# Kernel tuning notes

Measured on AMD Instinct MI355X. Metric: run time of the kernel, lower is better.

The kernel has to match this reference:

```python
import jax, jax.numpy as jnp
import numpy as np

F = 1024
H = 16
DH = F // H  # 64
MLP = 4096
EPS = 1e-5


def layernorm(x, g, b):
    mu = x.mean(-1, keepdims=True)
    var = ((x - mu) ** 2).mean(-1, keepdims=True)
    return (x - mu) * jax.lax.rsqrt(var + EPS) * g + b


def softmax_off_by_one(a):
    e = jnp.exp(a - a.max(-1, keepdims=True))
    return e / (1.0 + e.sum(-1, keepdims=True))


def setup_inputs() -> dict:
    key = jax.random.key(0)
    ks = jax.random.split(key, 12)
    s = 0.02
    return {
        "x": jax.random.normal(ks[0], (2, 2048, F), jnp.float32),
        "ln1_g": jnp.ones((F,), jnp.float32),
        "ln1_b": jnp.zeros((F,), jnp.float32),
        "Wq": jax.random.normal(ks[1], (F, F), jnp.float32) * s,
        "bq": jnp.zeros((F,), jnp.float32),
        "Wk": jax.random.normal(ks[2], (F, F), jnp.float32) * s,
        "bk": jnp.zeros((F,), jnp.float32),
        "Wv": jax.random.normal(ks[3], (F, F), jnp.float32) * s,
        "bv": jnp.zeros((F,), jnp.float32),
        "Wo": jax.random.normal(ks[4], (F, F), jnp.float32) * s,
        "bo": jnp.zeros((F,), jnp.float32),
        "slim": jnp.ones((H,), jnp.float32),
        "ln2_g": jnp.ones((F,), jnp.float32),
        "ln2_b": jnp.zeros((F,), jnp.float32),
        "W1": jax.random.normal(ks[5], (F, MLP), jnp.float32) * s,
        "b1": jnp.zeros((MLP,), jnp.float32),
        "W2": jax.random.normal(ks[6], (MLP, F), jnp.float32) * s,
        "b2": jnp.zeros((F,), jnp.float32),
    }


def reference(x, ln1_g, ln1_b, Wq, bq, Wk, bk, Wv, bv, Wo, bo, slim,
              ln2_g, ln2_b, W1, b1, W2, b2):
    b, n, f = x.shape
    h = layernorm(x, ln1_g, ln1_b)
    # project and split heads: [b, H, n, DH]
    q = (h @ Wq + bq).reshape(b, n, H, DH).transpose(0, 2, 1, 3)
    k = (h @ Wk + bk).reshape(b, n, H, DH).transpose(0, 2, 1, 3)
    v = (h @ Wv + bv).reshape(b, n, H, DH).transpose(0, 2, 1, 3)
    att = jnp.einsum('bhid,bhjd->bhij', q, k) / (DH ** 0.5)
    probs = softmax_off_by_one(att)  # off-by-one softmax
    probs = probs * slim[None, :, None, None]  # slimming after softmax
    attn = jnp.einsum('bhij,bhjd->bihd', probs, v).reshape(b, n, F)
    out = attn @ Wo + bo + x  # residual 1
    h2 = layernorm(out, ln2_g, ln2_b)
    m = jax.nn.gelu(h2 @ W1 + b1, approximate=False)
    m = jax.nn.gelu(m @ W2 + b2, approximate=False)
    return m + out  # residual 2
```

## Files before the change

### kernel.cpp

```cpp
#include <hip/hip_runtime.h>
#include <hip/hip_bf16.h>

typedef __hip_bfloat16 bf16;
typedef short bf16x8 __attribute__((ext_vector_type(8)));
typedef short bf16x4 __attribute__((ext_vector_type(4)));
typedef float f32x4 __attribute__((ext_vector_type(4)));

__device__ __forceinline__ float gelu_f(float x) {
  return 0.5f * x * (1.f + erff(x * 0.70710678118654752f));
}

__device__ __forceinline__ unsigned short f2bfu(float f) {
  bf16 h = __float2bfloat16(f);
  unsigned short u;
  __builtin_memcpy(&u, &h, 2);
  return u;
}

__device__ __forceinline__ void load16_lds(const bf16* g, bf16* l) {
  __builtin_amdgcn_global_load_lds(
      (const __attribute__((address_space(1))) unsigned int*)g,
      (__attribute__((address_space(3))) unsigned int*)l, 16, 0, 0);
}

__global__ __launch_bounds__(256) void transpose_cast(
    const float* __restrict__ src, bf16* __restrict__ dst, int R, int C) {
  __shared__ float tile[32][33];
  int tx = threadIdx.x & 31, ty = threadIdx.x >> 5;
  int r0 = blockIdx.y * 32, c0 = blockIdx.x * 32;
  #pragma unroll
  for (int i = ty; i < 32; i += 8)
    tile[i][tx] = src[(size_t)(r0 + i) * C + (c0 + tx)];
  __syncthreads();
  #pragma unroll
  for (int i = ty; i < 32; i += 8)
    dst[(size_t)(c0 + i) * R + (r0 + tx)] = __float2bfloat16(tile[tx][i]);
}

__global__ __launch_bounds__(256) void ln_kernel(
    const float* __restrict__ x, const float* __restrict__ g,
    const float* __restrict__ b, bf16* __restrict__ y) {
  int row = blockIdx.x;
  int t = threadIdx.x;
  const float4* xr = (const float4*)(x + (size_t)row * 1024);
  float4 v = xr[t];
  float s = v.x + v.y + v.z + v.w;
  float ss = v.x * v.x + v.y * v.y + v.z * v.z + v.w * v.w;
  #pragma unroll
  for (int off = 32; off >= 1; off >>= 1) {
    s += __shfl_xor(s, off);
    ss += __shfl_xor(ss, off);
  }
  __shared__ float red[8];
  int wv = t >> 6;
  if ((t & 63) == 0) { red[wv] = s; red[4 + wv] = ss; }
  __syncthreads();
  float S = red[0] + red[1] + red[2] + red[3];
  float SS = red[4] + red[5] + red[6] + red[7];
  float mu = S * (1.f / 1024.f);
  float var = SS * (1.f / 1024.f) - mu * mu;
  float inv = rsqrtf(var + 1e-5f);
  float4 gv = ((const float4*)g)[t];
  float4 bv = ((const float4*)b)[t];
  ushort4 o;
  o.x = f2bfu((v.x - mu) * inv * gv.x + bv.x);
  o.y = f2bfu((v.y - mu) * inv * gv.y + bv.y);
  o.z = f2bfu((v.z - mu) * inv * gv.z + bv.z);
  o.w = f2bfu((v.w - mu) * inv * gv.w + bv.w);
  ((ushort4*)(y + (size_t)row * 1024))[t] = o;
}

template <int EPI>
__global__ __launch_bounds__(256) void gemm_bf16(
    const bf16* __restrict__ A, const bf16* __restrict__ Bt,
    const float* __restrict__ bias0, const float* __restrict__ resid,
    void* __restrict__ C0, int M, int N, int K) {
  __shared__ __align__(16) bf16 As[2][128 * 32];
  __shared__ __align__(16) bf16 Bs[2][128 * 32];
  const int t = threadIdx.x, lane = t & 63, w = t >> 6;
  const int wm = (w >> 1) * 64, wn = (w & 1) * 64;
  const int m0 = blockIdx.y * 128, n0 = blockIdx.x * 128;

  const int srow = lane >> 2;
  const int sgrp = lane & 3;
  f32x4 acc[4][4] = {};

  const bf16* Abase = A + (size_t)m0 * K;
  const bf16* Bbase = Bt + (size_t)n0 * K;

  auto stage = [&](int buf, int kt) {
    #pragma unroll
    for (int c = 0; c < 2; ++c) {
      int row = w * 32 + c * 16 + srow;
      int sw = (row & 3) ^ ((row >> 2) & 3);
      int gg = sgrp ^ sw;
      const bf16* ga = Abase + (size_t)row * K + kt + gg * 8;
      const bf16* gb = Bbase + (size_t)row * K + kt + gg * 8;
      load16_lds(ga, &As[buf][(w * 32 + c * 16) * 32]);
      load16_lds(gb, &Bs[buf][(w * 32 + c * 16) * 32]);
    }
  };

  const int q8 = (((lane >> 4) ^ (lane & 3) ^ ((lane >> 2) & 3))) * 8;
  const int fr = lane & 15;

  const int nk = K >> 5;
  stage(0, 0);
  for (int i = 0; i < nk; ++i) {
    const int cur = i & 1;
    __syncthreads();
    if (i + 1 < nk) stage(cur ^ 1, (i + 1) << 5);
    bf16x8 af[4], bfr[4];
    #pragma unroll
    for (int mc = 0; mc < 4; ++mc)
      af[mc] = *(const bf16x8*)&As[cur][(wm + mc * 16 + fr) * 32 + q8];
    #pragma unroll
    for (int nc = 0; nc < 4; ++nc)
      bfr[nc] = *(const bf16x8*)&Bs[cur][(wn + nc * 16 + fr) * 32 + q8];
    #pragma unroll
    for (int mc = 0; mc < 4; ++mc)
      #pragma unroll
      for (int nc = 0; nc < 4; ++nc)
        acc[mc][nc] = __builtin_amdgcn_mfma_f32_16x16x32_bf16(
            af[mc], bfr[nc], acc[mc][nc], 0, 0, 0);
  }

  #pragma unroll
  for (int mc = 0; mc < 4; ++mc) {
    #pragma unroll
    for (int reg = 0; reg < 4; ++reg) {
      int m = m0 + wm + mc * 16 + ((lane >> 4) << 2) + reg;
      #pragma unroll
      for (int nc = 0; nc < 4; ++nc) {
        int n = n0 + wn + nc * 16 + (lane & 15);
        float val = acc[mc][nc][reg] + bias0[n];
        size_t idx = (size_t)m * N + n;
        if constexpr (EPI == 3) {
          ((float*)C0)[idx] = val + resid[idx];
        }
      }
    }
  }
}

template <int EPI>
__global__ __launch_bounds__(512, 2) void gemm256(
    const bf16* __restrict__ A, const bf16* __restrict__ Bt,
    const float* __restrict__ bias0, const float* __restrict__ bias1,
    const float* __restrict__ bias2,
    void* __restrict__ C0, void* __restrict__ C1, void* __restrict__ C2,
    int M, int N, int K) {
  __shared__ __align__(16) bf16 As[2][256 * 64];
  __shared__ __align__(16) bf16 Bs[2][256 * 64];
  const int t = threadIdx.x, lane = t & 63, w = t >> 6;
  const int wm = (w >> 2) * 128, wn = (w & 3) * 64;
  const int m0 = blockIdx.y * 256, n0 = blockIdx.x * 256;
  const int koff = (EPI == 6) ? (int)blockIdx.z * 1024 : 0;
  const int nk = ((EPI == 6) ? 1024 : K) >> 6;

  const bf16* Abase = A + (size_t)m0 * K + koff;
  const bf16* Bbase = Bt + (size_t)n0 * K + koff;

  const int lrow = lane >> 3;
  const int lgrp = (lane & 7) ^ lrow;
  const size_t lgoff = (size_t)lrow * K + lgrp * 8;

  auto stageA = [&](int buf, int half, int tile) {
    const int r = half * 128 + w * 16;
    const bf16* g = Abase + (size_t)r * K + tile * 64 + lgoff;
    bf16* l = &As[buf][r * 64];
    load16_lds(g, l);
    load16_lds(g + (size_t)8 * K, l + 8 * 64);
  };
  auto stageB = [&](int buf, int half, int tile) {
    const int r = half * 128 + w * 16;
    const bf16* g = Bbase + (size_t)r * K + tile * 64 + lgoff;
    bf16* l = &Bs[buf][r * 64];
    load16_lds(g, l);
    load16_lds(g + (size_t)8 * K, l + 8 * 64);
  };

  const int fr = lane & 15, qd = lane >> 4, frs = fr & 7;
  const int ao0 = (qd ^ frs) * 8;
  const int ao1 = ((4 + qd) ^ frs) * 8;
  const int rowA = (wm + fr) * 64;
  const int rowB = (wn + fr) * 64;

  f32x4 acc[8][4] = {};
  bf16x8 aF[8][2], bF[4][2];

#define MFMA_Q(MLO, NLO)                                                   \
  _Pragma("unroll")                                                        \
  for (int mi = (MLO); mi < (MLO) + 4; ++mi)                               \
    _Pragma("unroll")                                                      \
    for (int ni = (NLO); ni < (NLO) + 2; ++ni) {                           \
      acc[mi][ni] = __builtin_amdgcn_mfma_f32_16x16x32_bf16(               \
          aF[mi][0], bF[ni][0], acc[mi][ni], 0, 0, 0);                     \
      acc[mi][ni] = __builtin_amdgcn_mfma_f32_16x16x32_bf16(               \
          aF[mi][1], bF[ni][1], acc[mi][ni], 0, 0, 0);                     \
    }

  stageA(0, 0, 0); stageA(0, 1, 0); stageB(0, 0, 0); stageB(0, 1, 0);
  stageA(1, 0, 1);
  asm volatile("s_waitcnt vmcnt(6)" ::: "memory");
  asm volatile("s_barrier" ::: "memory");

  for (int i = 0; i < nk; ++i) {
    const int c = i & 1;
    const bf16* as = &As[c][0];
    const bf16* bs = &Bs[c][0];

    #pragma unroll
    for (int mi = 0; mi < 4; ++mi) {
      aF[mi][0] = *(const bf16x8*)(as + rowA + mi * 1024 + ao0);
      aF[mi][1] = *(const bf16x8*)(as + rowA + mi * 1024 + ao1);
    }
    if (i + 1 < nk) {
      stageA(c ^ 1, 1, i + 1);
      asm volatile("s_waitcnt vmcnt(4)" ::: "memory");
    } else {
      asm volatile("s_waitcnt vmcnt(0)" ::: "memory");
    }
    asm volatile("s_barrier" ::: "memory");
    __builtin_amdgcn_sched_barrier(0);
    if (i) {
      __builtin_amdgcn_s_setprio(1);
      MFMA_Q(4, 2)
      __builtin_amdgcn_s_setprio(0);
    }
    __builtin_amdgcn_sched_barrier(0);
    asm volatile("s_barrier" ::: "memory");

    #pragma unroll
    for (int ni = 0; ni < 2; ++ni) {
      bF[ni][0] = *(const bf16x8*)(bs + rowB + ni * 1024 + ao0);
      bF[ni][1] = *(const bf16x8*)(bs + rowB + ni * 1024 + ao1);
    }
    if (i + 1 < nk) stageB(c ^ 1, 0, i + 1);
    asm volatile("s_barrier" ::: "memory");
    asm volatile("s_waitcnt lgkmcnt(0)" ::: "memory");
    __builtin_amdgcn_sched_barrier(0);
    __builtin_amdgcn_s_setprio(1);
    MFMA_Q(0, 0)
    __builtin_amdgcn_s_setprio(0);
    __builtin_amdgcn_sched_barrier(0);
    asm volatile("s_barrier" ::: "memory");

    #pragma unroll
    for (int mi = 4; mi < 8; ++mi) {
      aF[mi][0] = *(const bf16x8*)(as + rowA + mi * 1024 + ao0);
      aF[mi][1] = *(const bf16x8*)(as + rowA + mi * 1024 + ao1);
    }
    if (i + 1 < nk) stageB(c ^ 1, 1, i + 1);
    asm volatile("s_barrier" ::: "memory");
    asm volatile("s_waitcnt lgkmcnt(0)" ::: "memory");
    __builtin_amdgcn_sched_barrier(0);
    __builtin_amdgcn_s_setprio(1);
    MFMA_Q(4, 0)
    __builtin_amdgcn_s_setprio(0);
    __builtin_amdgcn_sched_barrier(0);
    asm volatile("s_barrier" ::: "memory");

    #pragma unroll
    for (int ni = 2; ni < 4; ++ni) {
      bF[ni][0] = *(const bf16x8*)(bs + rowB + ni * 1024 + ao0);
      bF[ni][1] = *(const bf16x8*)(bs + rowB + ni * 1024 + ao1);
    }
    if (i + 2 < nk) stageA(c, 0, i + 2);
    if (i + 1 < nk) {
      if (i + 2 < nk) {
        asm volatile("s_waitcnt vmcnt(6)" ::: "memory");
      } else {
        asm volatile("s_waitcnt vmcnt(4)" ::: "memory");
      }
    }
    asm volatile("s_barrier" ::: "memory");
    asm volatile("s_waitcnt lgkmcnt(0)" ::: "memory");
    __builtin_amdgcn_sched_barrier(0);
    __builtin_amdgcn_s_setprio(1);
    MFMA_Q(0, 2)
    __builtin_amdgcn_s_setprio(0);
    __builtin_amdgcn_sched_barrier(0);
    asm volatile("s_barrier" ::: "memory");
  }
  MFMA_Q(4, 2)
#undef MFMA_Q

  if constexpr (EPI == 0) {
    const int which = n0 >> 10;
    const float* bp = which == 0 ? bias0 : which == 1 ? bias1 : bias2;
    bf16* qk = (bf16*)(which == 0 ? C0 : C1);
    const float qscale = 0.18033688011112042f;
    #pragma unroll
    for (int mi = 0; mi < 8; ++mi) {
      #pragma unroll
      for (int reg = 0; reg < 4; ++reg) {
        int m = m0 + wm + mi * 16 + qd * 4 + reg;
        int b = m >> 11, tok = m & 2047;
        #pragma unroll
        for (int ni = 0; ni < 4; ++ni) {
          int n = n0 + wn + ni * 16 + fr;
          int nn = n & 1023, hh = nn >> 6, d = n & 63;
          float val = acc[mi][ni][reg] + bp[nn];
          if (which == 2)
            ((bf16*)C2)[(size_t)((b * 16 + hh) * 64 + d) * 2048 + tok] =
                __float2bfloat16(val);
          else if (which == 0)
            qk[(size_t)((b * 16 + hh) * 2048 + tok) * 64 + d] =
                __float2bfloat16(val * qscale);
          else
            qk[(size_t)((b * 16 + hh) * 2048 + tok) * 64 + d] =
                __float2bfloat16(val);
        }
      }
    }
  } else if constexpr (EPI == 4) {
    #pragma unroll
    for (int mi = 0; mi < 8; ++mi) {
      #pragma unroll
      for (int reg = 0; reg < 4; ++reg) {
        int m = m0 + wm + mi * 16 + qd * 4 + reg;
        #pragma unroll
        for (int ni = 0; ni < 4; ++ni) {
          int n = n0 + wn + ni * 16 + fr;
          float val = acc[mi][ni][reg] + bias0[n];
          ((bf16*)C0)[(size_t)m * N + n] = __float2bfloat16(gelu_f(val));
        }
      }
    }
  } else {
    bf16* pout = (bf16*)C0 + (size_t)blockIdx.z * M * N;
    #pragma unroll
    for (int mi = 0; mi < 8; ++mi) {
      #pragma unroll
      for (int reg = 0; reg < 4; ++reg) {
        int m = m0 + wm + mi * 16 + qd * 4 + reg;
        #pragma unroll
        for (int ni = 0; ni < 4; ++ni) {
          int n = n0 + wn + ni * 16 + fr;
          pout[(size_t)m * N + n] = __float2bfloat16(acc[mi][ni][reg]);
        }
      }
    }
  }
}

__global__ __launch_bounds__(256) void reduce_mlp2(
    const bf16* __restrict__ part, const float* __restrict__ b2,
    const float* __restrict__ out1, float* __restrict__ out) {
  const int row = blockIdx.x, t = threadIdx.x;
  const size_t base = (size_t)row * 1024 + t * 4;
  float sum[4] = {0.f, 0.f, 0.f, 0.f};
  #pragma unroll
  for (int kc = 0; kc < 4; ++kc) {
    ushort4 u = *(const ushort4*)(part + (size_t)kc * 4096 * 1024 + base);
    unsigned short us[4] = {u.x, u.y, u.z, u.w};
    #pragma unroll
    for (int j = 0; j < 4; ++j) {
      bf16 h;
      __builtin_memcpy(&h, &us[j], 2);
      sum[j] += __bfloat162float(h);
    }
  }
  float4 bv = ((const float4*)b2)[t];
  float4 rv = *(const float4*)(out1 + base);
  float4 o;
  o.x = gelu_f(sum[0] + bv.x) + rv.x;
  o.y = gelu_f(sum[1] + bv.y) + rv.y;
  o.z = gelu_f(sum[2] + bv.z) + rv.z;
  o.w = gelu_f(sum[3] + bv.w) + rv.w;
  *(float4*)(out + base) = o;
}

__global__ __launch_bounds__(256) void attn_kernel(
    const bf16* __restrict__ q, const bf16* __restrict__ k,
    const bf16* __restrict__ vt, const float* __restrict__ slim,
    bf16* __restrict__ attn) {
  __shared__ __align__(16) bf16 Ks[64][72];
  __shared__ __align__(16) bf16 Vs[64][72];
  __shared__ __align__(16) bf16 Ps[4][2][16][72];

  const int t = threadIdx.x, lane = t & 63, w = t >> 6;
  const int fr = lane & 15, qd = lane >> 4;
  const int bh = blockIdx.y;
  const int q0 = blockIdx.x * 128;
  const size_t bhbase = (size_t)bh * 2048 * 64;

  bf16x8 qf[2][2];
  #pragma unroll
  for (int s = 0; s < 2; ++s) {
    const int qrow = q0 + s * 64 + w * 16 + fr;
    const bf16* qp = q + bhbase + (size_t)qrow * 64 + qd * 8;
    qf[s][0] = *(const bf16x8*)qp;
    qf[s][1] = *(const bf16x8*)(qp + 32);
  }

  const int r0 = t >> 3, g0 = t & 7;
  const bf16* kbase = k + bhbase + (size_t)r0 * 64 + g0 * 8;
  const bf16* vbase = vt + bhbase + (size_t)r0 * 2048 + g0 * 8;

  bf16x8 kreg0, kreg1, vreg0, vreg1;
  auto gload = [&](int j0) {
    kreg0 = *(const bf16x8*)(kbase + (size_t)j0 * 64);
    kreg1 = *(const bf16x8*)(kbase + (size_t)(j0 + 32) * 64);
    vreg0 = *(const bf16x8*)(vbase + j0);
    vreg1 = *(const bf16x8*)(vbase + (size_t)32 * 2048 + j0);
  };
  gload(0);

  f32x4 o_acc[2][4] = {};
  float m4[2][4] = {};
  float l4[2][4] = {};

  for (int it = 0; it < 32; ++it) {
    *(bf16x8*)&Ks[r0][g0 * 8] = kreg0;
    *(bf16x8*)&Ks[r0 + 32][g0 * 8] = kreg1;
    *(bf16x8*)&Vs[r0][g0 * 8] = vreg0;
    *(bf16x8*)&Vs[r0 + 32][g0 * 8] = vreg1;
    __syncthreads();
    if (it + 1 < 32) gload((it + 1) * 64);

    bf16x8 kf[4][2];
    #pragma unroll
    for (int nc = 0; nc < 4; ++nc) {
      int kr = nc * 16 + fr;
      kf[nc][0] = *(const bf16x8*)&Ks[kr][qd * 8];
      kf[nc][1] = *(const bf16x8*)&Ks[kr][32 + qd * 8];
    }

    f32x4 z[2][4];
    #pragma unroll
    for (int s = 0; s < 2; ++s)
      #pragma unroll
      for (int nc = 0; nc < 4; ++nc) {
        f32x4 zz = {};
        zz = __builtin_amdgcn_mfma_f32_16x16x32_bf16(kf[nc][0], qf[s][0], zz, 0, 0, 0);
        zz = __builtin_amdgcn_mfma_f32_16x16x32_bf16(kf[nc][1], qf[s][1], zz, 0, 0, 0);
        z[s][nc] = zz;
      }

    bf16x8 vf[4][2];
    #pragma unroll
    for (int dc = 0; dc < 4; ++dc) {
      int vr = dc * 16 + fr;
      vf[dc][0] = *(const bf16x8*)&Vs[vr][qd * 8];
      vf[dc][1] = *(const bf16x8*)&Vs[vr][32 + qd * 8];
    }

    #pragma unroll
    for (int s = 0; s < 2; ++s) {
      #pragma unroll
      for (int nc = 0; nc < 4; ++nc) {
        float p0 = __builtin_amdgcn_exp2f(z[s][nc][0]);
        float p1 = __builtin_amdgcn_exp2f(z[s][nc][1]);
        float p2 = __builtin_amdgcn_exp2f(z[s][nc][2]);
        float p3 = __builtin_amdgcn_exp2f(z[s][nc][3]);
        l4[s][nc] += (p0 + p1) + (p2 + p3);
        m4[s][nc] = fmaxf(m4[s][nc], fmaxf(fmaxf(p0, p1), fmaxf(p2, p3)));
        bf16x4 pk;
        pk[0] = (short)f2bfu(p0);
        pk[1] = (short)f2bfu(p1);
        pk[2] = (short)f2bfu(p2);
        pk[3] = (short)f2bfu(p3);
        *(bf16x4*)&Ps[w][s][fr][nc * 16 + qd * 4] = pk;
      }

      bf16x8 pf0 = *(const bf16x8*)&Ps[w][s][fr][qd * 8];
      bf16x8 pf1 = *(const bf16x8*)&Ps[w][s][fr][32 + qd * 8];
      #pragma unroll
      for (int dc = 0; dc < 4; ++dc) {
        o_acc[s][dc] = __builtin_amdgcn_mfma_f32_16x16x32_bf16(pf0, vf[dc][0], o_acc[s][dc], 0, 0, 0);
        o_acc[s][dc] = __builtin_amdgcn_mfma_f32_16x16x32_bf16(pf1, vf[dc][1], o_acc[s][dc], 0, 0, 0);
      }
    }
    __syncthreads();
  }

  const int b = bh >> 4, hh = bh & 15;
  const float sl = slim[hh];
  #pragma unroll
  for (int s = 0; s < 2; ++s) {
    float l_all = (l4[s][0] + l4[s][1]) + (l4[s][2] + l4[s][3]);
    float m_all = fmaxf(fmaxf(m4[s][0], m4[s][1]), fmaxf(m4[s][2], m4[s][3]));
    l_all += __shfl_xor(l_all, 16);
    m_all = fmaxf(m_all, __shfl_xor(m_all, 16));
    l_all += __shfl_xor(l_all, 32);
    m_all = fmaxf(m_all, __shfl_xor(m_all, 32));

    #pragma unroll
    for (int r = 0; r < 4; ++r) {
      float lr = __shfl(l_all, qd * 4 + r);
      float mr = __shfl(m_all, qd * 4 + r);
      float inv = sl / (mr + lr);
      int mrow = b * 2048 + q0 + s * 64 + w * 16 + qd * 4 + r;
      #pragma unroll
      for (int dc = 0; dc < 4; ++dc) {
        int col = hh * 64 + dc * 16 + fr;
        attn[(size_t)mrow * 1024 + col] = __float2bfloat16(o_acc[s][dc][r] * inv);
      }
    }
  }
}

extern "C" void kernel_launch(void* const* d_in, const int* in_sizes, int n_in,
                              void* d_out, int out_size, void* d_ws, size_t ws_size,
                              hipStream_t stream) {
  const float* x    = (const float*)d_in[0];
  const float* ln1g = (const float*)d_in[1];
  const float* ln1b = (const float*)d_in[2];
  const float* Wq   = (const float*)d_in[3];
  const float* bq   = (const float*)d_in[4];
  const float* Wk   = (const float*)d_in[5];
  const float* bk   = (const float*)d_in[6];
  const float* Wv   = (const float*)d_in[7];
  const float* bv   = (const float*)d_in[8];
  const float* Wo   = (const float*)d_in[9];
  const float* bo   = (const float*)d_in[10];
  const float* slim = (const float*)d_in[11];
  const float* ln2g = (const float*)d_in[12];
  const float* ln2b = (const float*)d_in[13];
  const float* W1   = (const float*)d_in[14];
  const float* b1   = (const float*)d_in[15];
  const float* W2   = (const float*)d_in[16];
  const float* b2   = (const float*)d_in[17];

  char* p = (char*)d_ws;
  auto take = [&](size_t nbytes) {
    char* r = p;
    p += (nbytes + 255) & ~(size_t)255;
    return r;
  };
  bf16* Wqkv_t = (bf16*)take((size_t)3072 * 1024 * 2);
  bf16* Wo_t = (bf16*)take((size_t)1024 * 1024 * 2);
  bf16* W1_t = (bf16*)take((size_t)4096 * 1024 * 2);
  bf16* W2_t = (bf16*)take((size_t)1024 * 4096 * 2);
  bf16* h1   = (bf16*)take((size_t)4096 * 1024 * 2);
  bf16* qb   = (bf16*)take((size_t)4096 * 1024 * 2);
  bf16* kb   = (bf16*)take((size_t)4096 * 1024 * 2);
  bf16* vtb  = (bf16*)take((size_t)4096 * 1024 * 2);
  bf16* attn = (bf16*)take((size_t)4096 * 1024 * 2);
  float* out1 = (float*)take((size_t)4096 * 1024 * 4);
  bf16* h2   = (bf16*)take((size_t)4096 * 1024 * 2);
  bf16* m1   = (bf16*)take((size_t)4096 * 4096 * 2);

  bf16* parts = h1;

  dim3 blk(256);
  dim3 blk512(512);

  transpose_cast<<<dim3(32, 32), blk, 0, stream>>>(Wq, Wqkv_t, 1024, 1024);
  transpose_cast<<<dim3(32, 32), blk, 0, stream>>>(Wk, Wqkv_t + (size_t)1024 * 1024, 1024, 1024);
  transpose_cast<<<dim3(32, 32), blk, 0, stream>>>(Wv, Wqkv_t + (size_t)2048 * 1024, 1024, 1024);
  transpose_cast<<<dim3(32, 32), blk, 0, stream>>>(Wo, Wo_t, 1024, 1024);
  transpose_cast<<<dim3(128, 32), blk, 0, stream>>>(W1, W1_t, 1024, 4096);
  transpose_cast<<<dim3(32, 128), blk, 0, stream>>>(W2, W2_t, 4096, 1024);

  ln_kernel<<<4096, blk, 0, stream>>>(x, ln1g, ln1b, h1);

  gemm256<0><<<dim3(12, 16), blk512, 0, stream>>>(
      h1, Wqkv_t, bq, bk, bv, qb, kb, vtb, 4096, 3072, 1024);

  attn_kernel<<<dim3(16, 32), blk, 0, stream>>>(qb, kb, vtb, slim, attn);

  gemm_bf16<3><<<dim3(8, 32), blk, 0, stream>>>(
      attn, Wo_t, bo, x, out1, 4096, 1024, 1024);

  ln_kernel<<<4096, blk, 0, stream>>>(out1, ln2g, ln2b, h2);

  gemm256<4><<<dim3(16, 16), blk512, 0, stream>>>(
      h2, W1_t, b1, nullptr, nullptr, m1, nullptr, nullptr, 4096, 4096, 1024);

  gemm256<6><<<dim3(4, 16, 4), blk512, 0, stream>>>(
      m1, W2_t, nullptr, nullptr, nullptr, parts, nullptr, nullptr,
      4096, 1024, 4096);
  reduce_mlp2<<<4096, blk, 0, stream>>>(parts, b2, out1, (float*)d_out);
}
```

Before: 406.3 us.

## Double-buffer K/V tiles via direct global-to-LDS loads with XOR swizzle

The attention kernel now stages K and V tiles straight from global memory into LDS with global_load_lds, using a two-slot ring so the next tile loads while the current one is being computed. It also drops one barrier per iteration and stops routing the data through registers. Row padding is replaced by an XOR chunk swizzle that keeps LDS reads conflict-free in the smaller layout. s_setprio is raised around the MFMA blocks so compute waves get issue priority. The risk is correctness if the async LDS writes are not fully waited on before the barrier.

```diff
diff --git a/kernel.cpp b/kernel.cpp
--- a/kernel.cpp
+++ b/kernel.cpp
@@ -376,8 +376,8 @@
     const bf16* __restrict__ q, const bf16* __restrict__ k,
     const bf16* __restrict__ vt, const float* __restrict__ slim,
     bf16* __restrict__ attn) {
-  __shared__ __align__(16) bf16 Ks[64][72];
-  __shared__ __align__(16) bf16 Vs[64][72];
+  __shared__ __align__(16) bf16 Ks[2][64][64];
+  __shared__ __align__(16) bf16 Vs[2][64][64];
   __shared__ __align__(16) bf16 Ps[4][2][16][72];
 
   const int t = threadIdx.x, lane = t & 63, w = t >> 6;
@@ -395,40 +395,44 @@
     qf[s][1] = *(const bf16x8*)(qp + 32);
   }
 
-  const int r0 = t >> 3, g0 = t & 7;
-  const bf16* kbase = k + bhbase + (size_t)r0 * 64 + g0 * 8;
-  const bf16* vbase = vt + bhbase + (size_t)r0 * 2048 + g0 * 8;
-
-  bf16x8 kreg0, kreg1, vreg0, vreg1;
-  auto gload = [&](int j0) {
-    kreg0 = *(const bf16x8*)(kbase + (size_t)j0 * 64);
-    kreg1 = *(const bf16x8*)(kbase + (size_t)(j0 + 32) * 64);
-    vreg0 = *(const bf16x8*)(vbase + j0);
-    vreg1 = *(const bf16x8*)(vbase + (size_t)32 * 2048 + j0);
+  const int rw = lane >> 3, sl = lane & 7;
+  const int gsw = (sl ^ rw) * 8;
+  auto stageKV = [&](int buf, int key0) {
+    #pragma unroll
+    for (int c = 0; c < 2; ++c) {
+      const int row0 = c * 32 + w * 8;
+      const bf16* gk = k + bhbase + (size_t)(key0 + row0 + rw) * 64 + gsw;
+      const bf16* gv = vt + bhbase + (size_t)(row0 + rw) * 2048 + key0 + gsw;
+      load16_lds(gk, &Ks[buf][row0][0]);
+      load16_lds(gv, &Vs[buf][row0][0]);
+    }
   };
-  gload(0);
+  stageKV(0, 0);
 
   f32x4 o_acc[2][4] = {};
   float m4[2][4] = {};
   float l4[2][4] = {};
 
+  const int frs = fr & 7;
+  const int so0 = (qd ^ frs) * 8;
+  const int so1 = ((4 + qd) ^ frs) * 8;
+
+  __syncthreads();
+
   for (int it = 0; it < 32; ++it) {
-    *(bf16x8*)&Ks[r0][g0 * 8] = kreg0;
-    *(bf16x8*)&Ks[r0 + 32][g0 * 8] = kreg1;
-    *(bf16x8*)&Vs[r0][g0 * 8] = vreg0;
-    *(bf16x8*)&Vs[r0 + 32][g0 * 8] = vreg1;
-    __syncthreads();
-    if (it + 1 < 32) gload((it + 1) * 64);
+    const int cur = it & 1;
+    if (it + 1 < 32) stageKV(cur ^ 1, (it + 1) * 64);
 
     bf16x8 kf[4][2];
     #pragma unroll
     for (int nc = 0; nc < 4; ++nc) {
-      int kr = nc * 16 + fr;
-      kf[nc][0] = *(const bf16x8*)&Ks[kr][qd * 8];
-      kf[nc][1] = *(const bf16x8*)&Ks[kr][32 + qd * 8];
+      const bf16* kr = &Ks[cur][nc * 16 + fr][0];
+      kf[nc][0] = *(const bf16x8*)(kr + so0);
+      kf[nc][1] = *(const bf16x8*)(kr + so1);
     }
 
     f32x4 z[2][4];
+    __builtin_amdgcn_s_setprio(1);
     #pragma unroll
     for (int s = 0; s < 2; ++s)
       #pragma unroll
@@ -438,13 +442,14 @@
         zz = __builtin_amdgcn_mfma_f32_16x16x32_bf16(kf[nc][1], qf[s][1], zz, 0, 0, 0);
         z[s][nc] = zz;
       }
+    __builtin_amdgcn_s_setprio(0);
 
     bf16x8 vf[4][2];
     #pragma unroll
     for (int dc = 0; dc < 4; ++dc) {
-      int vr = dc * 16 + fr;
-      vf[dc][0] = *(const bf16x8*)&Vs[vr][qd * 8];
-      vf[dc][1] = *(const bf16x8*)&Vs[vr][32 + qd * 8];
+      const bf16* vr = &Vs[cur][dc * 16 + fr][0];
+      vf[dc][0] = *(const bf16x8*)(vr + so0);
+      vf[dc][1] = *(const bf16x8*)(vr + so1);
     }
 
     #pragma unroll
@@ -467,17 +472,19 @@
 
       bf16x8 pf0 = *(const bf16x8*)&Ps[w][s][fr][qd * 8];
       bf16x8 pf1 = *(const bf16x8*)&Ps[w][s][fr][32 + qd * 8];
+      __builtin_amdgcn_s_setprio(1);
       #pragma unroll
       for (int dc = 0; dc < 4; ++dc) {
         o_acc[s][dc] = __builtin_amdgcn_mfma_f32_16x16x32_bf16(pf0, vf[dc][0], o_acc[s][dc], 0, 0, 0);
         o_acc[s][dc] = __builtin_amdgcn_mfma_f32_16x16x32_bf16(pf1, vf[dc][1], o_acc[s][dc], 0, 0, 0);
       }
+      __builtin_amdgcn_s_setprio(0);
     }
     __syncthreads();
   }
 
   const int b = bh >> 4, hh = bh & 15;
-  const float sl = slim[hh];
+  const float sl_f = slim[hh];
   #pragma unroll
   for (int s = 0; s < 2; ++s) {
     float l_all = (l4[s][0] + l4[s][1]) + (l4[s][2] + l4[s][3]);
@@ -491,7 +498,7 @@
     for (int r = 0; r < 4; ++r) {
       float lr = __shfl(l_all, qd * 4 + r);
       float mr = __shfl(m_all, qd * 4 + r);
-      float inv = sl / (mr + lr);
+      float inv = sl_f / (mr + lr);
       int mrow = b * 2048 + q0 + s * 64 + w * 16 + qd * 4 + r;
       #pragma unroll
       for (int dc = 0; dc < 4; ++dc) {
```

Result: slower. 417.5 us (+2.8%).

## Load K/V fragments directly from global into registers, dropping LDS staging

Applied to the files above, without the earlier changes.

The attention kernel stops staging K and V tiles through shared memory with block-wide barriers. Each wave now loads its MFMA operand fragments straight from global memory into double-buffered registers, and the next tile's K and V loads are issued around the current tile's matrix ops. It also adds s_setprio around the MFMA sections and sets launch bounds to one block per SM. The goal is to remove LDS round trips and __syncthreads stalls. The cost is that each of the four waves now fetches the same K/V data from global/L2 redundantly, and register pressure rises, which may lower occupancy.

```diff
diff --git a/kernel.cpp b/kernel.cpp
--- a/kernel.cpp
+++ b/kernel.cpp
@@ -372,12 +372,10 @@
   *(float4*)(out + base) = o;
 }
 
-__global__ __launch_bounds__(256) void attn_kernel(
+__global__ __launch_bounds__(256, 1) void attn_kernel(
     const bf16* __restrict__ q, const bf16* __restrict__ k,
     const bf16* __restrict__ vt, const float* __restrict__ slim,
     bf16* __restrict__ attn) {
-  __shared__ __align__(16) bf16 Ks[64][72];
-  __shared__ __align__(16) bf16 Vs[64][72];
   __shared__ __align__(16) bf16 Ps[4][2][16][72];
 
   const int t = threadIdx.x, lane = t & 63, w = t >> 6;
@@ -395,89 +393,93 @@
     qf[s][1] = *(const bf16x8*)(qp + 32);
   }
 
-  const int r0 = t >> 3, g0 = t & 7;
-  const bf16* kbase = k + bhbase + (size_t)r0 * 64 + g0 * 8;
-  const bf16* vbase = vt + bhbase + (size_t)r0 * 2048 + g0 * 8;
-
-  bf16x8 kreg0, kreg1, vreg0, vreg1;
-  auto gload = [&](int j0) {
-    kreg0 = *(const bf16x8*)(kbase + (size_t)j0 * 64);
-    kreg1 = *(const bf16x8*)(kbase + (size_t)(j0 + 32) * 64);
-    vreg0 = *(const bf16x8*)(vbase + j0);
-    vreg1 = *(const bf16x8*)(vbase + (size_t)32 * 2048 + j0);
-  };
-  gload(0);
+  const bf16* kfb = k + bhbase + (size_t)fr * 64 + qd * 8;
+  const bf16* vfb = vt + bhbase + (size_t)fr * 2048 + qd * 8;
+
+  bf16x8 kR[2][4][2], vR[2][4][2];
+
+#define ISSUE_K(SL, KEY0)                                                     \
+  _Pragma("unroll")                                                           \
+  for (int nc = 0; nc < 4; ++nc) {                                            \
+    const bf16* kp_ = kfb + (size_t)((KEY0) + nc * 16) * 64;                  \
+    kR[SL][nc][0] = *(const bf16x8*)kp_;                                      \
+    kR[SL][nc][1] = *(const bf16x8*)(kp_ + 32);                               \
+  }
+
+#define ISSUE_V(SL, KEY0)                                                     \
+  _Pragma("unroll")                                                           \
+  for (int dc = 0; dc < 4; ++dc) {                                            \
+    const bf16* vp_ = vfb + (size_t)dc * 16 * 2048 + (KEY0);                  \
+    vR[SL][dc][0] = *(const bf16x8*)vp_;                                      \
+    vR[SL][dc][1] = *(const bf16x8*)(vp_ + 32);                               \
+  }
 
   f32x4 o_acc[2][4] = {};
   float m4[2][4] = {};
   float l4[2][4] = {};
 
-  for (int it = 0; it < 32; ++it) {
-    *(bf16x8*)&Ks[r0][g0 * 8] = kreg0;
-    *(bf16x8*)&Ks[r0 + 32][g0 * 8] = kreg1;
-    *(bf16x8*)&Vs[r0][g0 * 8] = vreg0;
-    *(bf16x8*)&Vs[r0 + 32][g0 * 8] = vreg1;
-    __syncthreads();
-    if (it + 1 < 32) gload((it + 1) * 64);
-
-    bf16x8 kf[4][2];
-    #pragma unroll
-    for (int nc = 0; nc < 4; ++nc) {
-      int kr = nc * 16 + fr;
-      kf[nc][0] = *(const bf16x8*)&Ks[kr][qd * 8];
-      kf[nc][1] = *(const bf16x8*)&Ks[kr][32 + qd * 8];
-    }
-
-    f32x4 z[2][4];
-    #pragma unroll
-    for (int s = 0; s < 2; ++s)
-      #pragma unroll
-      for (int nc = 0; nc < 4; ++nc) {
-        f32x4 zz = {};
-        zz = __builtin_amdgcn_mfma_f32_16x16x32_bf16(kf[nc][0], qf[s][0], zz, 0, 0, 0);
-        zz = __builtin_amdgcn_mfma_f32_16x16x32_bf16(kf[nc][1], qf[s][1], zz, 0, 0, 0);
-        z[s][nc] = zz;
-      }
-
-    bf16x8 vf[4][2];
-    #pragma unroll
-    for (int dc = 0; dc < 4; ++dc) {
-      int vr = dc * 16 + fr;
-      vf[dc][0] = *(const bf16x8*)&Vs[vr][qd * 8];
-      vf[dc][1] = *(const bf16x8*)&Vs[vr][32 + qd * 8];
-    }
-
-    #pragma unroll
-    for (int s = 0; s < 2; ++s) {
-      #pragma unroll
-      for (int nc = 0; nc < 4; ++nc) {
-        float p0 = __builtin_amdgcn_exp2f(z[s][nc][0]);
-        float p1 = __builtin_amdgcn_exp2f(z[s][nc][1]);
-        float p2 = __builtin_amdgcn_exp2f(z[s][nc][2]);
-        float p3 = __builtin_amdgcn_exp2f(z[s][nc][3]);
-        l4[s][nc] += (p0 + p1) + (p2 + p3);
-        m4[s][nc] = fmaxf(m4[s][nc], fmaxf(fmaxf(p0, p1), fmaxf(p2, p3)));
-        bf16x4 pk;
-        pk[0] = (short)f2bfu(p0);
-        pk[1] = (short)f2bfu(p1);
-        pk[2] = (short)f2bfu(p2);
-        pk[3] = (short)f2bfu(p3);
-        *(bf16x4*)&Ps[w][s][fr][nc * 16 + qd * 4] = pk;
-      }
-
-      bf16x8 pf0 = *(const bf16x8*)&Ps[w][s][fr][qd * 8];
-      bf16x8 pf1 = *(const bf16x8*)&Ps[w][s][fr][32 + qd * 8];
-      #pragma unroll
-      for (int dc = 0; dc < 4; ++dc) {
-        o_acc[s][dc] = __builtin_amdgcn_mfma_f32_16x16x32_bf16(pf0, vf[dc][0], o_acc[s][dc], 0, 0, 0);
-        o_acc[s][dc] = __builtin_amdgcn_mfma_f32_16x16x32_bf16(pf1, vf[dc][1], o_acc[s][dc], 0, 0, 0);
-      }
-    }
-    __syncthreads();
-  }
+  ISSUE_K(0, 0)
+  ISSUE_V(0, 0)
+
+#define ITER_BODY(CUR, NXT, IT)                                               \
+  {                                                                           \
+    if ((IT) + 1 < 32) { ISSUE_K(NXT, ((IT) + 1) * 64) }                      \
+    f32x4 z[2][4];                                                            \
+    __builtin_amdgcn_s_setprio(1);                                            \
+    _Pragma("unroll")                                                         \
+    for (int s = 0; s < 2; ++s)                                               \
+      _Pragma("unroll")                                                       \
+      for (int nc = 0; nc < 4; ++nc) {                                        \
+        f32x4 zz = {};                                                        \
+        zz = __builtin_amdgcn_mfma_f32_16x16x32_bf16(kR[CUR][nc][0],          \
+                                                     qf[s][0], zz, 0, 0, 0);  \
+        zz = __builtin_amdgcn_mfma_f32_16x16x32_bf16(kR[CUR][nc][1],          \
+                                                     qf[s][1], zz, 0, 0, 0);  \
+        z[s][nc] = zz;                                                        \
+      }                                                                       \
+    __builtin_amdgcn_s_setprio(0);                                            \
+    if ((IT) + 1 < 32) { ISSUE_V(NXT, ((IT) + 1) * 64) }                      \
+    _Pragma("unroll")                                                         \
+    for (int s = 0; s < 2; ++s) {                                             \
+      _Pragma("unroll")                                                       \
+      for (int nc = 0; nc < 4; ++nc) {                                        \
+        float p0 = __builtin_amdgcn_exp2f(z[s][nc][0]);                       \
+        float p1 = __builtin_amdgcn_exp2f(z[s][nc][1]);                       \
+        float p2 = __builtin_amdgcn_exp2f(z[s][nc][2]);                       \
+        float p3 = __builtin_amdgcn_exp2f(z[s][nc][3]);                       \
+        l4[s][nc] += (p0 + p1) + (p2 + p3);                                   \
+        m4[s][nc] = fmaxf(m4[s][nc], fmaxf(fmaxf(p0, p1), fmaxf(p2, p3)));    \
+        bf16x4 pk;                                                            \
+        pk[0] = (short)f2bfu(p0);                                             \
+        pk[1] = (short)f2bfu(p1);                                             \
+        pk[2] = (short)f2bfu(p2);                                             \
+        pk[3] = (short)f2bfu(p3);                                             \
+        *(bf16x4*)&Ps[w][s][fr][nc * 16 + qd * 4] = pk;                       \
+      }                                                                       \
+      bf16x8 pf0 = *(const bf16x8*)&Ps[w][s][fr][qd * 8];                     \
+      bf16x8 pf1 = *(const bf16x8*)&Ps[w][s][fr][32 + qd * 8];                \
+      __builtin_amdgcn_s_setprio(1);                                          \
+      _Pragma("unroll")                                                       \
+      for (int dc = 0; dc < 4; ++dc) {                                        \
+        o_acc[s][dc] = __builtin_amdgcn_mfma_f32_16x16x32_bf16(               \
+            pf0, vR[CUR][dc][0], o_acc[s][dc], 0, 0, 0);                      \
+        o_acc[s][dc] = __builtin_amdgcn_mfma_f32_16x16x32_bf16(               \
+            pf1, vR[CUR][dc][1], o_acc[s][dc], 0, 0, 0);                      \
+      }                                                                       \
+      __builtin_amdgcn_s_setprio(0);                                          \
+    }                                                                         \
+  }
+
+  for (int it = 0; it < 32; it += 2) {
+    ITER_BODY(0, 1, it)
+    ITER_BODY(1, 0, it + 1)
+  }
+#undef ITER_BODY
+#undef ISSUE_K
+#undef ISSUE_V
 
   const int b = bh >> 4, hh = bh & 15;
-  const float sl = slim[hh];
+  const float sl_f = slim[hh];
   #pragma unroll
   for (int s = 0; s < 2; ++s) {
     float l_all = (l4[s][0] + l4[s][1]) + (l4[s][2] + l4[s][3]);
@@ -491,7 +493,7 @@
     for (int r = 0; r < 4; ++r) {
       float lr = __shfl(l_all, qd * 4 + r);
       float mr = __shfl(m_all, qd * 4 + r);
-      float inv = sl / (mr + lr);
+      float inv = sl_f / (mr + lr);
       int mrow = b * 2048 + q0 + s * 64 + w * 16 + qd * 4 + r;
       #pragma unroll
       for (int dc = 0; dc < 4; ++dc) {
```

Measured after the change: 464.8 us. 1.14x slower.
